# Performance work log

Measured on AMD Instinct MI355X. Metric: run time of the kernel, lower is better.

Reference implementation:

```python
import jax, jax.numpy as jnp
import numpy as np

B, N, C = 16, 1024, 768
NUM_HEADS = 8
HEAD_DIM = C // NUM_HEADS
TEMP_INIT = 0.05
EPS_NORM = 1e-12   # F.normalize eps
EPS_LN = 1e-5      # LayerNorm eps


def setup_inputs() -> dict:
    key = jax.random.key(0)
    ks = jax.random.split(key, 4)
    x = jax.random.normal(ks[0], (B, N, C), dtype=jnp.float32)
    w_qkv = jax.random.normal(ks[1], (3 * C, C), dtype=jnp.float32) * (1.0 / np.sqrt(C))
    w_proj = jax.random.normal(ks[2], (C, C), dtype=jnp.float32) * (1.0 / np.sqrt(C))
    temperature = jnp.ones((NUM_HEADS, 1, 1), dtype=jnp.float32) * TEMP_INIT
    conv_w = jax.random.normal(ks[3], (C, 1, 3, 3), dtype=jnp.float32) * (1.0 / 3.0)
    gamma = jnp.ones((C,), dtype=jnp.float32)
    beta = jnp.zeros((C,), dtype=jnp.float32)
    return {"x": x, "w_qkv": w_qkv, "w_proj": w_proj, "temperature": temperature,
            "conv_w": conv_w, "gamma": gamma, "beta": beta, "H": 32, "W": 32}


def _l2norm_tokens(t):
    # normalize along token dim (axis=-2), matching F.normalize(dim=-2)
    n = jnp.sqrt(jnp.sum(t * t, axis=-2, keepdims=True))
    return t / jnp.maximum(n, EPS_NORM)


def reference(x, w_qkv, w_proj, temperature, conv_w, gamma, beta, H, W):
    b, n, c = x.shape
    h, d = NUM_HEADS, HEAD_DIM
    qkv = (x @ w_qkv.T).reshape(b, n, 3, h, d).transpose(2, 0, 3, 1, 4)  # [3,B,h,N,d]
    q, k, v = qkv[0], qkv[1], qkv[2]
    q = _l2norm_tokens(q)
    k = _l2norm_tokens(k)
    # cross-covariance attention over channels: [B,h,d,d]
    A = jnp.einsum('bhnd,bhne->bhde', q, k) / temperature[None]
    A = jax.nn.softmax(A, axis=-1)
    # v @ A^T : [B,h,N,d]
    x_xca = jnp.einsum('bhne,bhde->bhnd', v, A)
    x_xca = x_xca.transpose(0, 2, 1, 3).reshape(b, n, c)
    x_xca = x_xca @ w_proj.T
    # depthwise 3x3 local propagation
    x_img = x.transpose(0, 2, 1).reshape(b, c, H, W)
    x_local = jax.lax.conv_general_dilated(
        x_img, conv_w, window_strides=(1, 1), padding=((1, 1), (1, 1)),
        dimension_numbers=('NCHW', 'OIHW', 'NCHW'), feature_group_count=c)
    x_local = x_local.reshape(b, c, n).transpose(0, 2, 1)
    y = x_xca + 0.1 * x_local
    mu = jnp.mean(y, axis=-1, keepdims=True)
    var = jnp.mean((y - mu) ** 2, axis=-1, keepdims=True)
    return (y - mu) * jax.lax.rsqrt(var + EPS_LN) * gamma + beta
```

## Files before the change

kernel.cpp:

```cpp
#include <hip/hip_runtime.h>

#define DEVI __device__ __forceinline__

typedef __bf16 bf16x8 __attribute__((ext_vector_type(8)));
typedef float f32x4 __attribute__((ext_vector_type(4)));

DEVI unsigned short f2bf(float f) {
  unsigned u = __builtin_bit_cast(unsigned, f);
  u += 0x7FFFu + ((u >> 16) & 1u);
  return (unsigned short)(u >> 16);
}
DEVI float bf2f(unsigned short s) {
  return __builtin_bit_cast(float, ((unsigned)s) << 16);
}
DEVI f32x4 mfma16(bf16x8 a, bf16x8 b, f32x4 c) {
  return __builtin_amdgcn_mfma_f32_16x16x32_bf16(a, b, c, 0, 0, 0);
}
DEVI void gload16(const void* g, void* l) {
  __builtin_amdgcn_global_load_lds(
      (const __attribute__((address_space(1))) void*)g,
      (__attribute__((address_space(3))) void*)l, 16, 0, 0);
}
template <int ROWB>
DEVI bf16x8 frag_ld(const char* lds, int row, int kb) {
  int off = row * ROWB + (kb ^ ((row & 7) << 4));
  return __builtin_bit_cast(bf16x8, *(const uint4*)(lds + off));
}

__global__ __launch_bounds__(256) void k_cvt2(const float* __restrict__ a,
                                              unsigned short* __restrict__ oa, int n4a,
                                              const float* __restrict__ b,
                                              unsigned short* __restrict__ ob, int n4b) {
  const int tid = threadIdx.x;
  if (blockIdx.x < 1792) {
    for (int i = blockIdx.x * 256 + tid; i < n4a; i += 1792 * 256) {
      float4 f = ((const float4*)a)[i];
      ushort4 o;
      o.x = f2bf(f.x); o.y = f2bf(f.y); o.z = f2bf(f.z); o.w = f2bf(f.w);
      ((ushort4*)oa)[i] = o;
    }
  } else {
    for (int i = (blockIdx.x - 1792) * 256 + tid; i < n4b; i += 256 * 256) {
      float4 f = ((const float4*)b)[i];
      ushort4 o;
      o.x = f2bf(f.x); o.y = f2bf(f.y); o.z = f2bf(f.z); o.w = f2bf(f.w);
      ((ushort4*)ob)[i] = o;
    }
  }
}

template <int MODE>
DEVI void gemm_body(char* lds, const unsigned short* __restrict__ A,
                    const unsigned short* __restrict__ B0,
                    unsigned short* __restrict__ o0, unsigned short* __restrict__ o1,
                    unsigned short* __restrict__ o2) {
  const int tid = threadIdx.x, l = tid & 63, wid = tid >> 6;
  const int wr = wid >> 2, wc = wid & 3;
  const int xg = blockIdx.x;
  const int CPX = MODE ? 64 : 192;
  const int NJT = MODE ? 4 : 12;
  const int li = (xg & 7) * CPX + (xg >> 3);
  const int jt = li % NJT, mt = li / NJT;
  const int m0 = mt * 128, j0 = jt * 192;
  const unsigned short* Bb = MODE ? B0 + (size_t)(m0 >> 10) * 589824 : B0;

  const unsigned short* srcg[4][2];
  int ldso[4][2];
#pragma unroll
  for (int sg = 0; sg < 4; ++sg) {
    const bool isA = (sg == 0) || (sg == 3);
#pragma unroll
    for (int i = 0; i < 2; ++i) {
      int c;
      if (sg == 0)      c = (wid < 4) ? wid : wid + 4;
      else if (sg == 3) c = (wid < 4) ? wid + 4 : wid + 8;
      else if (sg == 1) { int cc = 2 * wid + i; c = (cc >> 2) * 6 + (cc & 3); }
      else              c = (wid >> 1) * 6 + 4 + (wid & 1);
      const int r0 = 8 * c;
      const int r = r0 + (l >> 3);
      const int scol = ((l & 7) ^ (l >> 3)) << 3;
      srcg[sg][i] = (isA ? A + (size_t)(m0 + r) * 768 : Bb + (size_t)(j0 + r) * 768) + scol;
      ldso[sg][i] = (isA ? 0 : 16384) + r0 * 128;
    }
  }
  const int swz = (l & 7) << 4;
  const int uu = (l >> 4) << 4;
  const int c0 = uu ^ swz;
  const int c1 = (64 | uu) ^ swz;
  const int arow = (wr * 64 + (l & 15)) * 128;
  const int brow = 16384 + (wc * 48 + (l & 15)) * 128;

  f32x4 acc[4][3];
#pragma unroll
  for (int i = 0; i < 4; ++i)
#pragma unroll
    for (int j = 0; j < 3; ++j)
#pragma unroll
      for (int e = 0; e < 4; ++e) acc[i][j][e] = 0.f;
  bf16x8 a[2][2], a2[2][2], b01[2][2], b2[2];

#define STAGE1(sg, nxt, ko) \
  gload16(srcg[sg][0] + (ko), lds + (nxt)*40960 + ldso[sg][0])
#define STAGE2(sg, nxt, ko)                                        \
  do {                                                             \
    gload16(srcg[sg][0] + (ko), lds + (nxt)*40960 + ldso[sg][0]);  \
    gload16(srcg[sg][1] + (ko), lds + (nxt)*40960 + ldso[sg][1]);  \
  } while (0)
#define LD128(off) __builtin_bit_cast(bf16x8, *(const uint4*)(cb_ + (off)))

  STAGE1(0, 0, 0); STAGE2(1, 0, 0); STAGE1(2, 0, 0); STAGE1(3, 0, 0);
  asm volatile("s_waitcnt vmcnt(2)" ::: "memory");
  __builtin_amdgcn_s_barrier();

#define KBODY(KT, LASTF)                                                              \
  {                                                                                   \
    const char* cb_ = lds + ((KT) & 1) * 40960;                                       \
    const int nxt = (((KT) & 1) ^ 1);                                                 \
    const int ko = ((KT) + 1) * 64;                                                   \
                           \
    _Pragma("unroll") for (int mf = 0; mf < 2; ++mf) {                                \
      a[mf][0] = LD128(arow + mf * 2048 + c0);                                        \
      a[mf][1] = LD128(arow + mf * 2048 + c1);                                        \
    }                                                                                 \
    _Pragma("unroll") for (int nf = 0; nf < 2; ++nf) {                                \
      b01[nf][0] = LD128(brow + nf * 2048 + c0);                                      \
      b01[nf][1] = LD128(brow + nf * 2048 + c1);                                      \
    }                                                                                 \
    if (!(LASTF)) {                                                                   \
      STAGE1(0, nxt, ko); STAGE2(1, nxt, ko);                                         \
      asm volatile("s_waitcnt vmcnt(3)" ::: "memory");                                \
    } else {                                                                          \
      asm volatile("s_waitcnt vmcnt(0)" ::: "memory");                                \
    }                                                                                 \
    __builtin_amdgcn_s_barrier();                                                     \
    __builtin_amdgcn_s_setprio(1);                                                    \
    _Pragma("unroll") for (int mf = 0; mf < 2; ++mf)                                  \
      _Pragma("unroll") for (int nf = 0; nf < 2; ++nf) {                              \
        acc[mf][nf] = mfma16(a[mf][0], b01[nf][0], acc[mf][nf]);                      \
        acc[mf][nf] = mfma16(a[mf][1], b01[nf][1], acc[mf][nf]);                      \
      }                                                                               \
    __builtin_amdgcn_s_setprio(0);                                                    \
              \
    b2[0] = LD128(brow + 2 * 2048 + c0);                                              \
    b2[1] = LD128(brow + 2 * 2048 + c1);                                              \
    _Pragma("unroll") for (int mf = 0; mf < 2; ++mf) {                                \
      a2[mf][0] = LD128(arow + (mf + 2) * 2048 + c0);                                 \
      a2[mf][1] = LD128(arow + (mf + 2) * 2048 + c1);                                 \
    }                                                                                 \
    if (!(LASTF)) {                                                                   \
      STAGE1(2, nxt, ko); STAGE1(3, nxt, ko);                                         \
      asm volatile("s_waitcnt vmcnt(2)" ::: "memory");                                \
    }                                                                                 \
    __builtin_amdgcn_s_barrier();                                                     \
    __builtin_amdgcn_s_setprio(1);                                                    \
    _Pragma("unroll") for (int mf = 0; mf < 2; ++mf) {                                \
      acc[mf][2] = mfma16(a[mf][0], b2[0], acc[mf][2]);                               \
      acc[mf][2] = mfma16(a[mf][1], b2[1], acc[mf][2]);                               \
    }                                                                                 \
    _Pragma("unroll") for (int mf = 0; mf < 2; ++mf)                                  \
      _Pragma("unroll") for (int nf = 0; nf < 2; ++nf) {                              \
        acc[mf + 2][nf] = mfma16(a2[mf][0], b01[nf][0], acc[mf + 2][nf]);             \
        acc[mf + 2][nf] = mfma16(a2[mf][1], b01[nf][1], acc[mf + 2][nf]);             \
      }                                                                               \
    _Pragma("unroll") for (int mf = 0; mf < 2; ++mf) {                                \
      acc[mf + 2][2] = mfma16(a2[mf][0], b2[0], acc[mf + 2][2]);                      \
      acc[mf + 2][2] = mfma16(a2[mf][1], b2[1], acc[mf + 2][2]);                      \
    }                                                                                 \
    __builtin_amdgcn_s_setprio(0);                                                    \
  }

#pragma unroll 1
  for (int kt = 0; kt < 11; ++kt) KBODY(kt, false);
  KBODY(11, true);
#undef KBODY
#undef STAGE2
#undef STAGE1
#undef LD128

  if constexpr (MODE == 0) {
    const int s = j0 / 768;
    const int jin0 = (j0 % 768) + wc * 48 + (l & 15);
    const int ntok0 = m0 + wr * 64 + ((l >> 4) << 2);
#pragma unroll
    for (int mf = 0; mf < 4; ++mf) {
      const int nt = ntok0 + mf * 16;
      const int bb = nt >> 10, nin = nt & 1023;
#pragma unroll
      for (int nf = 0; nf < 3; ++nf) {
        const int jj = jin0 + nf * 16;
        const int hh = jj / 96, dd = jj % 96;
        if (s == 2) {
          unsigned short* vp = o2 + (size_t)nt * 768 + jj;
#pragma unroll
          for (int rr = 0; rr < 4; ++rr) vp[rr * 768] = f2bf(acc[mf][nf][rr]);
        } else {
          unsigned short* base = (s == 0) ? o0 : o1;
          ushort4 pk;
          pk.x = f2bf(acc[mf][nf][0]); pk.y = f2bf(acc[mf][nf][1]);
          pk.z = f2bf(acc[mf][nf][2]); pk.w = f2bf(acc[mf][nf][3]);
          *(ushort4*)(base + ((size_t)((bb * 8 + hh) * 96 + dd)) * 1024 + nin) = pk;
        }
      }
    }
  } else {
    const int ntok0 = m0 + wr * 64 + ((l >> 4) << 2);
    const int col0 = j0 + wc * 48 + (l & 15);
#pragma unroll
    for (int mf = 0; mf < 4; ++mf)
#pragma unroll
      for (int nf = 0; nf < 3; ++nf) {
        unsigned short* yp = o0 + (size_t)(ntok0 + mf * 16) * 768 + col0 + nf * 16;
#pragma unroll
        for (int rr = 0; rr < 4; ++rr) yp[rr * 768] = f2bf(acc[mf][nf][rr]);
      }
  }
}

__global__ __launch_bounds__(512, 4) void kg0_qkv(const unsigned short* __restrict__ A,
                                                  const unsigned short* __restrict__ B0,
                                                  unsigned short* __restrict__ o0,
                                                  unsigned short* __restrict__ o1,
                                                  unsigned short* __restrict__ o2) {
  __shared__ alignas(16) char lds[81920];
  gemm_body<0>(lds, A, B0, o0, o1, o2);
}
__global__ __launch_bounds__(512, 4) void kg1_proj(const unsigned short* __restrict__ A,
                                                   const unsigned short* __restrict__ B0,
                                                   unsigned short* __restrict__ o0) {
  __shared__ alignas(16) char lds[81920];
  gemm_body<1>(lds, A, B0, o0, nullptr, nullptr);
}

DEVI float ssq8(uint4 u) {
  unsigned a[4] = {u.x, u.y, u.z, u.w};
  float s = 0.f;
#pragma unroll
  for (int i = 0; i < 4; ++i) {
    float lo = __builtin_bit_cast(float, a[i] << 16);
    float hi = __builtin_bit_cast(float, a[i] & 0xFFFF0000u);
    s += lo * lo + hi * hi;
  }
  return s;
}

__global__ __launch_bounds__(256) void k_attn(const unsigned short* __restrict__ qT,
                                              const unsigned short* __restrict__ kT,
                                              const float* __restrict__ temp,
                                              unsigned short* __restrict__ PT) {
  __shared__ alignas(16) char lQK[2][24576];
  __shared__ float lA[96 * 96];
  __shared__ float lrq[96], lrk[96];
  const int bh = blockIdx.x, tid = threadIdx.x, lane = tid & 63, wid = tid >> 6;
  const float invt = 1.f / temp[bh & 7];
  const int wr = wid >> 1, wc = wid & 1;
  const unsigned short* qb = qT + (size_t)bh * 96 * 1024;
  const unsigned short* kb = kT + (size_t)bh * 96 * 1024;

  const unsigned short* srcp[6];
  int dsto[6];
#pragma unroll
  for (int i = 0; i < 6; ++i) {
    int cid = wid * 6 + i;
    bool isK = cid >= 12;
    int c = isK ? cid - 12 : cid;
    int p = c * 1024 + lane * 16;
    int r = p >> 7, cb = p & 127;
    int cbs = cb ^ ((r & 7) << 4);
    srcp[i] = (isK ? kb : qb) + (size_t)r * 1024 + (cbs >> 1);
    dsto[i] = (isK ? 12288 : 0) + c * 1024;
  }

#pragma unroll
  for (int i = 0; i < 6; ++i) gload16(srcp[i], lQK[0] + dsto[i]);

  for (int row = wid; row < 192; row += 4) {
    const unsigned short* src = (row < 96) ? qb + (size_t)row * 1024
                                           : kb + (size_t)(row - 96) * 1024;
    const uint4* p = (const uint4*)src + lane * 2;
    float s = ssq8(p[0]) + ssq8(p[1]);
#pragma unroll
    for (int off = 32; off; off >>= 1) s += __shfl_xor(s, off, 64);
    if (lane == 0) {
      float r = 1.f / fmaxf(sqrtf(s), 1e-12f);
      if (row < 96) lrq[row] = r;
      else          lrk[row - 96] = r;
    }
  }

  f32x4 acc[3][3];
#pragma unroll
  for (int i = 0; i < 3; ++i)
#pragma unroll
    for (int j = 0; j < 3; ++j)
#pragma unroll
      for (int e = 0; e < 4; ++e) acc[i][j][e] = 0.f;

  asm volatile("s_waitcnt vmcnt(0)" ::: "memory");
  __builtin_amdgcn_s_barrier();

#pragma unroll 1
  for (int kt = 0; kt < 16; ++kt) {
    const char* bq = lQK[kt & 1];
    if (kt < 15) {
      char* nb = lQK[(kt + 1) & 1];
      const int ko = (kt + 1) * 64;
#pragma unroll
      for (int i = 0; i < 6; ++i) gload16(srcp[i] + ko, nb + dsto[i]);
    }
#pragma unroll
    for (int ks = 0; ks < 2; ++ks) {
      const int kb2 = ks * 64 + ((lane >> 4) << 4);
      bf16x8 af[3], bfv[3];
#pragma unroll
      for (int mb = 0; mb < 3; ++mb) af[mb] = frag_ld<128>(bq, wr * 48 + mb * 16 + (lane & 15), kb2);
#pragma unroll
      for (int nb2 = 0; nb2 < 3; ++nb2) bfv[nb2] = frag_ld<128>(bq + 12288, wc * 48 + nb2 * 16 + (lane & 15), kb2);
#pragma unroll
      for (int mb = 0; mb < 3; ++mb)
#pragma unroll
        for (int nb2 = 0; nb2 < 3; ++nb2) acc[mb][nb2] = mfma16(af[mb], bfv[nb2], acc[mb][nb2]);
    }
    asm volatile("s_waitcnt vmcnt(0)" ::: "memory");
    __builtin_amdgcn_s_barrier();
  }

  const int rb = wr * 48 + ((lane >> 4) << 2);
  const int eb = wc * 48 + (lane & 15);
#pragma unroll
  for (int mb = 0; mb < 3; ++mb)
#pragma unroll
    for (int nb = 0; nb < 3; ++nb) {
      int e = eb + nb * 16;
#pragma unroll
      for (int rr = 0; rr < 4; ++rr) {
        int d = rb + mb * 16 + rr;
        lA[d * 96 + e] = acc[mb][nb][rr] * lrq[d] * lrk[e] * invt;
      }
    }
  __syncthreads();
  for (int d = wid; d < 96; d += 4) {
    float v0 = lA[d * 96 + lane];
    float v1 = (lane < 32) ? lA[d * 96 + 64 + lane] : -3.0e38f;
    float mx = fmaxf(v0, v1);
#pragma unroll
    for (int off = 32; off; off >>= 1) mx = fmaxf(mx, __shfl_xor(mx, off, 64));
    float p0 = __expf(v0 - mx);
    float p1 = (lane < 32) ? __expf(v1 - mx) : 0.f;
    float ssum = p0 + p1;
#pragma unroll
    for (int off = 32; off; off >>= 1) ssum += __shfl_xor(ssum, off, 64);
    float rs = 1.f / ssum;
    PT[((size_t)bh * 96 + lane) * 96 + d] = f2bf(p0 * rs);
    if (lane < 32) PT[((size_t)bh * 96 + 64 + lane) * 96 + d] = f2bf(p1 * rs);
  }
}

__global__ __launch_bounds__(256) void k_prep(const unsigned short* __restrict__ PT,
                                              const float* __restrict__ wproj,
                                              unsigned short* __restrict__ B_all) {
  __shared__ alignas(16) char pl[19968 + 39936];
  unsigned short* lPt = (unsigned short*)pl;
  unsigned short* lW  = (unsigned short*)(pl + 19968);
  unsigned short* tr  = lW;
  const int blk = blockIdx.x;
  const int b = blk >> 5, h = (blk >> 2) & 7, cq = blk & 3;
  const int tid = threadIdx.x, l = tid & 63, wid = tid >> 6;
  const int wr = wid >> 1, wc = wid & 1;

  const unsigned short* pt = PT + (size_t)(b * 8 + h) * 96 * 96;
  for (int idx = tid; idx < 1152; idx += 256) {
    int r = idx / 12, ch = idx % 12;
    *(uint4*)(lPt + r * 104 + ch * 8) = *(const uint4*)(pt + r * 96 + ch * 8);
  }
  for (int idx = tid; idx < 4608; idx += 256) {
    int r = idx / 24, ch = idx % 24;
    float4 f = *(const float4*)(wproj + (size_t)(cq * 192 + r) * 768 + h * 96 + ch * 4);
    ushort4 o;
    o.x = f2bf(f.x); o.y = f2bf(f.y); o.z = f2bf(f.z); o.w = f2bf(f.w);
    *(ushort4*)(lW + r * 104 + ch * 4) = o;
  }
  __syncthreads();

  f32x4 acc[3][6];
#pragma unroll
  for (int i = 0; i < 3; ++i)
#pragma unroll
    for (int j = 0; j < 6; ++j)
#pragma unroll
      for (int e = 0; e < 4; ++e) acc[i][j][e] = 0.f;

#pragma unroll
  for (int ks = 0; ks < 3; ++ks) {
    const int kof = ks * 32 + ((l >> 4) << 3);
    bf16x8 af[3], bv[6];
#pragma unroll
    for (int mb = 0; mb < 3; ++mb)
      af[mb] = __builtin_bit_cast(bf16x8, *(const uint4*)(lPt + (wr * 48 + mb * 16 + (l & 15)) * 104 + kof));
#pragma unroll
    for (int nb = 0; nb < 6; ++nb)
      bv[nb] = __builtin_bit_cast(bf16x8, *(const uint4*)(lW + (wc * 96 + nb * 16 + (l & 15)) * 104 + kof));
#pragma unroll
    for (int mb = 0; mb < 3; ++mb)
#pragma unroll
      for (int nb = 0; nb < 6; ++nb) acc[mb][nb] = mfma16(af[mb], bv[nb], acc[mb][nb]);
  }

  __syncthreads();
  const int e0 = wr * 48 + ((l >> 4) << 2);
  const int cl0 = wc * 96 + (l & 15);
#pragma unroll
  for (int mb = 0; mb < 3; ++mb)
#pragma unroll
    for (int nb = 0; nb < 6; ++nb) {
      ushort4 pk;
      pk.x = f2bf(acc[mb][nb][0]); pk.y = f2bf(acc[mb][nb][1]);
      pk.z = f2bf(acc[mb][nb][2]); pk.w = f2bf(acc[mb][nb][3]);
      *(ushort4*)(tr + (cl0 + nb * 16) * 100 + e0 + mb * 16) = pk;
    }
  __syncthreads();
  for (int idx = tid; idx < 2304; idx += 256) {
    int r = idx / 12, ch = idx % 12;
    uint4 u = *(const uint4*)(tr + r * 100 + ch * 8);
    *(uint4*)(B_all + ((size_t)(b * 768) + cq * 192 + r) * 768 + h * 96 + ch * 8) = u;
  }
}

__global__ __launch_bounds__(256) void k_final(const unsigned short* __restrict__ yp,
                                               const unsigned short* __restrict__ xb16,
                                               const float* __restrict__ cw,
                                               const float* __restrict__ gamma,
                                               const float* __restrict__ beta,
                                               float* __restrict__ out) {
  const int wid = threadIdx.x >> 6, lane = threadIdx.x & 63;
  const int m = blockIdx.x * 4 + wid;
  const int bb = m >> 10, n = m & 1023, yy = n >> 5, xx = n & 31;
  const unsigned short* xb = xb16 + (size_t)bb * 1024 * 768;

  float yv[3][4];
#pragma unroll
  for (int g = 0; g < 3; ++g) {
    const int c = g * 256 + lane * 4;
    float w36[36];
    const float4* wp = (const float4*)(cw + (size_t)c * 9);
#pragma unroll
    for (int i = 0; i < 9; ++i) *(float4*)(w36 + i * 4) = wp[i];

    float a0 = 0.f, a1 = 0.f, a2 = 0.f, a3 = 0.f;
#pragma unroll
    for (int dy = -1; dy <= 1; ++dy) {
      int ny = yy + dy;
      if ((unsigned)ny < 32u) {
#pragma unroll
        for (int dx = -1; dx <= 1; ++dx) {
          int nx = xx + dx;
          if ((unsigned)nx < 32u) {
            ushort4 v = *(const ushort4*)(xb + (size_t)(ny * 32 + nx) * 768 + c);
            const int j = (dy + 1) * 3 + (dx + 1);
            a0 += w36[0 * 9 + j] * bf2f(v.x);
            a1 += w36[1 * 9 + j] * bf2f(v.y);
            a2 += w36[2 * 9 + j] * bf2f(v.z);
            a3 += w36[3 * 9 + j] * bf2f(v.w);
          }
        }
      }
    }
    ushort4 f = *(const ushort4*)(yp + (size_t)m * 768 + c);
    yv[g][0] = bf2f(f.x) + 0.1f * a0;
    yv[g][1] = bf2f(f.y) + 0.1f * a1;
    yv[g][2] = bf2f(f.z) + 0.1f * a2;
    yv[g][3] = bf2f(f.w) + 0.1f * a3;
  }

  float s1 = 0.f, s2 = 0.f;
#pragma unroll
  for (int g = 0; g < 3; ++g)
#pragma unroll
    for (int e = 0; e < 4; ++e) { s1 += yv[g][e]; s2 += yv[g][e] * yv[g][e]; }
#pragma unroll
  for (int off = 32; off; off >>= 1) {
    s1 += __shfl_xor(s1, off, 64);
    s2 += __shfl_xor(s2, off, 64);
  }
  const float mu = s1 * (1.f / 768.f);
  const float var = s2 * (1.f / 768.f) - mu * mu;
  const float rs = rsqrtf(var + 1e-5f);

#pragma unroll
  for (int g = 0; g < 3; ++g) {
    const int c = g * 256 + lane * 4;
    float4 gm = *(const float4*)(gamma + c);
    float4 bt = *(const float4*)(beta + c);
    float4 o;
    o.x = (yv[g][0] - mu) * rs * gm.x + bt.x;
    o.y = (yv[g][1] - mu) * rs * gm.y + bt.y;
    o.z = (yv[g][2] - mu) * rs * gm.z + bt.z;
    o.w = (yv[g][3] - mu) * rs * gm.w + bt.w;
    *(float4*)(out + (size_t)m * 768 + c) = o;
  }
}

extern "C" void kernel_launch(void* const* d_in, const int* in_sizes, int n_in,
                              void* d_out, int out_size, void* d_ws, size_t ws_size,
                              hipStream_t stream) {
  const float* x     = (const float*)d_in[0];
  const float* wqkv  = (const float*)d_in[1];
  const float* wproj = (const float*)d_in[2];
  const float* temp  = (const float*)d_in[3];
  const float* cw    = (const float*)d_in[4];
  const float* gamma = (const float*)d_in[5];
  const float* beta  = (const float*)d_in[6];
  float* out = (float*)d_out;
  char* ws = (char*)d_ws;

  unsigned short* xb    = (unsigned short*)(ws);
  unsigned short* wqb   = (unsigned short*)(ws + 25165824);
  unsigned short* qT    = (unsigned short*)(ws + 28704768);
  unsigned short* yp    = qT;
  unsigned short* kT    = (unsigned short*)(ws + 53870592);
  unsigned short* B_all = kT;
  unsigned short* vP    = (unsigned short*)(ws + 79036416);
  unsigned short* PT    = (unsigned short*)(ws + 104202240);

  k_cvt2<<<dim3(2048), dim3(256), 0, stream>>>(x, xb, 16384 * 768 / 4,
                                               wqkv, wqb, 2304 * 768 / 4);
  kg0_qkv<<<dim3(1536), dim3(512), 0, stream>>>(xb, wqb, qT, kT, vP);
  k_attn<<<dim3(128), dim3(256), 0, stream>>>(qT, kT, temp, PT);
  k_prep<<<dim3(512), dim3(256), 0, stream>>>(PT, wproj, B_all);
  kg1_proj<<<dim3(512), dim3(512), 0, stream>>>(vP, B_all, yp);
  k_final<<<dim3(4096), dim3(256), 0, stream>>>(yp, xb, cw, gamma, beta, out);
}
```

Baseline: 230.5 us.

## Remap block indices so each XCD handles contiguous data slices across kernels

Result: no change. 230.2 us (-0.1%).

```diff
diff --git a/kernel.cpp b/kernel.cpp
--- a/kernel.cpp
+++ b/kernel.cpp
@@ -32,15 +32,17 @@
                                               const float* __restrict__ b,
                                               unsigned short* __restrict__ ob, int n4b) {
   const int tid = threadIdx.x;
-  if (blockIdx.x < 1792) {
-    for (int i = blockIdx.x * 256 + tid; i < n4a; i += 1792 * 256) {
+  if (blockIdx.x < 2048) {
+    const int chunk = (blockIdx.x & 7) * 256 + (blockIdx.x >> 3);
+    const int i0 = chunk * 1536;
+    for (int i = i0 + tid; i < i0 + 1536; i += 256) {
       float4 f = ((const float4*)a)[i];
       ushort4 o;
       o.x = f2bf(f.x); o.y = f2bf(f.y); o.z = f2bf(f.z); o.w = f2bf(f.w);
       ((ushort4*)oa)[i] = o;
     }
   } else {
-    for (int i = (blockIdx.x - 1792) * 256 + tid; i < n4b; i += 256 * 256) {
+    for (int i = (blockIdx.x - 2048) * 256 + tid; i < n4b; i += 256 * 256) {
       float4 f = ((const float4*)b)[i];
       ushort4 o;
       o.x = f2bf(f.x); o.y = f2bf(f.y); o.z = f2bf(f.z); o.w = f2bf(f.w);
@@ -250,8 +252,12 @@
   __shared__ alignas(16) char lQK[2][24576];
   __shared__ float lA[96 * 96];
   __shared__ float lrq[96], lrk[96];
-  const int bh = blockIdx.x, tid = threadIdx.x, lane = tid & 63, wid = tid >> 6;
-  const float invt = 1.f / temp[bh & 7];
+  const int blk = blockIdx.x, tid = threadIdx.x, lane = tid & 63, wid = tid >> 6;
+  const int idx = blk >> 3;
+  const int bb = (blk & 7) * 2 + (idx >> 3);
+  const int hh = idx & 7;
+  const int bh = bb * 8 + hh;
+  const float invt = 1.f / temp[hh];
   const int wr = wid >> 1, wc = wid & 1;
   const unsigned short* qb = qT + (size_t)bh * 96 * 1024;
   const unsigned short* kb = kT + (size_t)bh * 96 * 1024;
@@ -363,17 +369,19 @@
   unsigned short* lW  = (unsigned short*)(pl + 19968);
   unsigned short* tr  = lW;
   const int blk = blockIdx.x;
-  const int b = blk >> 5, h = (blk >> 2) & 7, cq = blk & 3;
+  const int idx = blk >> 3;
+  const int b = (blk & 7) * 2 + (idx >> 5);
+  const int h = (idx >> 2) & 7, cq = idx & 3;
   const int tid = threadIdx.x, l = tid & 63, wid = tid >> 6;
   const int wr = wid >> 1, wc = wid & 1;
 
   const unsigned short* pt = PT + (size_t)(b * 8 + h) * 96 * 96;
-  for (int idx = tid; idx < 1152; idx += 256) {
-    int r = idx / 12, ch = idx % 12;
+  for (int i2 = tid; i2 < 1152; i2 += 256) {
+    int r = i2 / 12, ch = i2 % 12;
     *(uint4*)(lPt + r * 104 + ch * 8) = *(const uint4*)(pt + r * 96 + ch * 8);
   }
-  for (int idx = tid; idx < 4608; idx += 256) {
-    int r = idx / 24, ch = idx % 24;
+  for (int i2 = tid; i2 < 4608; i2 += 256) {
+    int r = i2 / 24, ch = i2 % 24;
     float4 f = *(const float4*)(wproj + (size_t)(cq * 192 + r) * 768 + h * 96 + ch * 4);
     ushort4 o;
     o.x = f2bf(f.x); o.y = f2bf(f.y); o.z = f2bf(f.z); o.w = f2bf(f.w);
@@ -418,8 +426,8 @@
       *(ushort4*)(tr + (cl0 + nb * 16) * 100 + e0 + mb * 16) = pk;
     }
   __syncthreads();
-  for (int idx = tid; idx < 2304; idx += 256) {
-    int r = idx / 12, ch = idx % 12;
+  for (int i2 = tid; i2 < 2304; i2 += 256) {
+    int r = i2 / 12, ch = i2 % 12;
     uint4 u = *(const uint4*)(tr + r * 100 + ch * 8);
     *(uint4*)(B_all + ((size_t)(b * 768) + cq * 192 + r) * 768 + h * 96 + ch * 8) = u;
   }
@@ -432,7 +440,7 @@
                                                const float* __restrict__ beta,
                                                float* __restrict__ out) {
   const int wid = threadIdx.x >> 6, lane = threadIdx.x & 63;
-  const int m = blockIdx.x * 4 + wid;
+  const int m = (blockIdx.x & 7) * 2048 + (blockIdx.x >> 3) * 4 + wid;
   const int bb = m >> 10, n = m & 1023, yy = n >> 5, xx = n & 31;
   const unsigned short* xb = xb16 + (size_t)bb * 1024 * 768;
 
@@ -521,7 +529,7 @@
   unsigned short* vP    = (unsigned short*)(ws + 79036416);
   unsigned short* PT    = (unsigned short*)(ws + 104202240);
 
-  k_cvt2<<<dim3(2048), dim3(256), 0, stream>>>(x, xb, 16384 * 768 / 4,
+  k_cvt2<<<dim3(2304), dim3(256), 0, stream>>>(x, xb, 16384 * 768 / 4,
                                                wqkv, wqb, 2304 * 768 / 4);
   kg0_qkv<<<dim3(1536), dim3(512), 0, stream>>>(xb, wqb, qT, kT, vP);
   k_attn<<<dim3(128), dim3(256), 0, stream>>>(qT, kT, temp, PT);
```
